# Optimization experiments

Measured on AMD Instinct MI355X. Metric: run time of the kernel, lower is better.

## Reference

```python
import jax, jax.numpy as jnp
import numpy as np

N = 1_000_000
BS = 4
SPATIAL_SHAPE = np.array([480.0, 360.0, 32.0], dtype=np.float32)
SCALES = [2, 4, 8, 16, 1]  # scale_list + [1]
POL_MIN = np.array([0.0, -3.14159265, -4.0], dtype=np.float32)
POL_MAX = np.array([50.0, 3.14159265, 2.0], dtype=np.float32)


def setup_inputs() -> dict:
    key = jax.random.key(0)
    kxy, kz, ki, kb = jax.random.split(key, 4)
    xy = jax.random.uniform(kxy, (N, 2), jnp.float32, -35.0, 35.0)   # rho <= 49.5 < 50
    z = jax.random.uniform(kz, (N, 1), jnp.float32, -4.0, 2.0)
    inten = jax.random.uniform(ki, (N, 1), jnp.float32)
    points = jnp.concatenate([xy, z, inten], axis=1)                  # [N, 4]
    batch_idx = jax.random.randint(kb, (N,), 0, BS, jnp.int64)
    return {"points": points, "batch_idx": batch_idx}


def _cart2polar(xyz):
    rho = jnp.sqrt(xyz[:, 0] ** 2 + xyz[:, 1] ** 2)
    phi = jnp.arctan2(xyz[:, 1], xyz[:, 0])
    return jnp.stack([rho, phi, xyz[:, 2]], axis=1)  # [N, 3]


def reference(points, batch_idx):
    pc = points[:, :3]
    pol = _cart2polar(pc)                                            # [N, 3]
    minb = jnp.asarray(POL_MIN)
    crop = jnp.asarray(POL_MAX - POL_MIN)
    b = batch_idx.astype(jnp.int64)

    outputs = []
    for scale in SCALES:
        ss_np = np.ceil(SPATIAL_SHAPE / scale)                       # static per-scale grid
        ss = jnp.asarray(ss_np, dtype=pol.dtype)
        # quantize: spatial_shape * (pol - min) / crop, truncated like torch .long()
        idx = (ss * (pol - minb) / crop).astype(jnp.int64)           # [N, 3] nonneg in-range
        x, y, z = idx[:, 0], idx[:, 1], idx[:, 2]
        bxyz_indx = jnp.stack([b, x, y, z], axis=-1)                 # full_coors [N, 4]
        # encode row -> single int64 key for sort-based unique (strides = shape+1)
        sx, sy, sz = (np.int64(s) + 1 for s in ss_np)
        key = ((b * sx + x) * sy + y) * sz + z
        unq_key, unq_inv = jnp.unique(
            key, return_inverse=True, size=N, fill_value=-1
        )
        # decode padded unique keys back to (b, x, y, z); pad rows decode from -1
        uz = unq_key % sz
        t = unq_key // sz
        uy = t % sy
        t = t // sy
        ux = t % sx
        ub = t // sx
        coors = jnp.stack([ub, uz, uy, ux], axis=1).astype(jnp.int32)  # [b, z, y, x]
        outputs.extend([bxyz_indx, unq_inv.reshape(-1), coors])
    return tuple(outputs)
```

## Files before the change

### kernel.cpp

```cpp
#include <hip/hip_runtime.h>

#define NPTS 1000000
#define OUT_STRIDE (9 * NPTS)

constexpr int   kSX[5]  = {241, 121, 61, 31, 481};
constexpr int   kSY[5]  = {181,  91, 46, 24, 361};
constexpr int   kSZ[5]  = { 17,   9,  5,  3,  33};
constexpr float kSSX[5] = {240.f, 120.f, 60.f, 30.f, 480.f};
constexpr float kSSY[5] = {180.f,  90.f, 45.f, 23.f, 360.f};
constexpr float kSSZ[5] = { 16.f,   8.f,  4.f,  2.f,  32.f};
constexpr int kWB[5] = {0, 92736, 105152, 106944, 107264};
#define W_TOTAL 823552
#define SCAN_BLOCKS 403

#define BM_BYTES ((size_t)W_TOTAL * 32)
#define BM_U4    (BM_BYTES / 16)

#define SCAT_BLOCKS 3217
#define PAD_BLOCKS  19532
#define INV_BLOCKS  3907
#define EMIT_BLOCKS (SCAT_BLOCKS + PAD_BLOCKS + INV_BLOCKS)

__global__ void zero_kernel(uint4* __restrict__ p) {
  size_t i = (size_t)blockIdx.x * 256 + threadIdx.x;
  if (i < BM_U4) p[i] = make_uint4(0u, 0u, 0u, 0u);
}

__global__ void mark_kernel(const float4* __restrict__ pts,
                            const int* __restrict__ bidx,
                            int* __restrict__ out,
                            unsigned char* __restrict__ bytemap) {
  int i = blockIdx.x * 256 + threadIdx.x;
  if (i >= NPTS) return;
  float4 p = pts[i];
  float rho = __fsqrt_rn(__fadd_rn(__fmul_rn(p.x, p.x), __fmul_rn(p.y, p.y)));
  float phi = (float)atan2((double)p.y, (double)p.x);
  float zz = p.z;
  int b = bidx[i];
  const float PI_F = 3.14159265f;
  const float CROP1 = PI_F + PI_F;
#pragma unroll
  for (int s = 0; s < 5; ++s) {
    int ix = (int)__fdiv_rn(__fmul_rn(kSSX[s], rho), 50.0f);
    int iy = (int)__fdiv_rn(__fmul_rn(kSSY[s], __fsub_rn(phi, -PI_F)), CROP1);
    int iz = (int)__fdiv_rn(__fmul_rn(kSSZ[s], __fsub_rn(zz, -4.0f)), 6.0f);
    int key = ((b * kSX[s] + ix) * kSY[s] + iy) * kSZ[s] + iz;
    ((int4*)(out + (size_t)s * OUT_STRIDE))[i] = make_int4(b, ix, iy, iz);
    bytemap[(size_t)kWB[s] * 32 + (unsigned)key] = 1;
  }
}

__device__ __forceinline__ unsigned nib(unsigned u) {
  return (u | (u >> 7) | (u >> 14) | (u >> 21)) & 0xFu;
}
__device__ __forceinline__ unsigned word_from_bytes(const uint4* p) {
  uint4 a = p[0], b = p[1];
  return nib(a.x) | (nib(a.y) << 4) | (nib(a.z) << 8) | (nib(a.w) << 12) |
         (nib(b.x) << 16) | (nib(b.y) << 20) | (nib(b.z) << 24) | (nib(b.w) << 28);
}

__global__ void scan1_kernel(const uint4* __restrict__ bytemap,
                             unsigned* __restrict__ bits,
                             unsigned* __restrict__ wp,
                             unsigned* __restrict__ bsums) {
  __shared__ unsigned sh[256];
  int tid = threadIdx.x;
  int base = blockIdx.x * 2048 + tid * 8;
  unsigned c[8];
  unsigned sum = 0;
#pragma unroll
  for (int j = 0; j < 8; ++j) {
    c[j] = sum;
    int w = base + j;
    unsigned m = 0;
    if (w < W_TOTAL) {
      m = word_from_bytes(bytemap + (size_t)w * 2);
      bits[w] = m;
    }
    sum += (unsigned)__popc(m);
  }
  sh[tid] = sum;
  __syncthreads();
  for (int off = 1; off < 256; off <<= 1) {
    unsigned v = (tid >= off) ? sh[tid - off] : 0u;
    __syncthreads();
    sh[tid] += v;
    __syncthreads();
  }
  unsigned tbase = sh[tid] - sum;
#pragma unroll
  for (int j = 0; j < 8; ++j) {
    int w = base + j;
    if (w < W_TOTAL) wp[w] = tbase + c[j];
  }
  if (tid == 0) bsums[blockIdx.x] = sh[255];
}

__global__ void scan2_kernel(unsigned* __restrict__ bsums) {
  __shared__ unsigned sh[1024];
  int t = threadIdx.x;
  unsigned v = (t < SCAN_BLOCKS) ? bsums[t] : 0u;
  sh[t] = v;
  __syncthreads();
  for (int off = 1; off < 1024; off <<= 1) {
    unsigned u = (t >= off) ? sh[t - off] : 0u;
    __syncthreads();
    sh[t] += u;
    __syncthreads();
  }
  if (t < SCAN_BLOCKS) bsums[t] = sh[t] - v;
  if (t == SCAN_BLOCKS - 1) bsums[512] = sh[t];
}

__device__ __forceinline__ unsigned fullp(const unsigned* wp, const unsigned* bs, int w) {
  return wp[w] + bs[w >> 11];
}

__device__ __forceinline__ unsigned region_count(int s, const unsigned* wp,
                                                 const unsigned* bs) {
  unsigned lo = fullp(wp, bs, kWB[s]);
  unsigned hi = (s == 4) ? bs[512] : fullp(wp, bs, kWB[s + 1]);
  return hi - lo;
}

__global__ void emit_kernel(const float4* __restrict__ pts,
                            const int* __restrict__ bidx,
                            const unsigned* __restrict__ bits,
                            const unsigned* __restrict__ wp,
                            const unsigned* __restrict__ bsums,
                            int* __restrict__ out) {
  int blk = blockIdx.x;
  if (blk < SCAT_BLOCKS) {
    int w = blk * 256 + threadIdx.x;
    if (w >= W_TOTAL) return;
    unsigned word = bits[w];
    if (!word) return;
    int s, wb;
    unsigned sx, sy, sz;
    if      (w >= kWB[4]) { s = 4; wb = kWB[4]; sx = 481; sy = 361; sz = 33; }
    else if (w >= kWB[3]) { s = 3; wb = kWB[3]; sx = 31;  sy = 24;  sz = 3;  }
    else if (w >= kWB[2]) { s = 2; wb = kWB[2]; sx = 61;  sy = 46;  sz = 5;  }
    else if (w >= kWB[1]) { s = 1; wb = kWB[1]; sx = 121; sy = 91;  sz = 9;  }
    else                  { s = 0; wb = 0;      sx = 241; sy = 181; sz = 17; }
    unsigned rank = fullp(wp, bsums, w) - fullp(wp, bsums, wb);
    int4* coors = (int4*)(out + (size_t)s * OUT_STRIDE + 5 * NPTS);
    unsigned kbase = (unsigned)(w - wb) * 32u;
    while (word) {
      int bit = __ffs(word) - 1;
      word &= word - 1;
      unsigned k = kbase + (unsigned)bit;
      unsigned z = k % sz; unsigned t = k / sz;
      unsigned y = t % sy; t /= sy;
      unsigned x = t % sx; unsigned b = t / sx;
      coors[rank++] = make_int4((int)b, (int)z, (int)y, (int)x);
    }
  } else if (blk < SCAT_BLOCKS + PAD_BLOCKS) {
    int idx = (blk - SCAT_BLOCKS) * 256 + threadIdx.x;
    if (idx >= 5 * NPTS) return;
    int s = idx / NPTS;
    int r = idx - s * NPTS;
    unsigned uniq = region_count(s, wp, bsums);
    if ((unsigned)r < uniq) return;
    ((int4*)(out + (size_t)s * OUT_STRIDE + 5 * NPTS))[r] =
        make_int4(-1, kSZ[s] - 1, kSY[s] - 1, kSX[s] - 1);
  } else {
    int i = (blk - SCAT_BLOCKS - PAD_BLOCKS) * 256 + threadIdx.x;
    if (i >= NPTS) return;
    float4 p = pts[i];
    float rho = __fsqrt_rn(__fadd_rn(__fmul_rn(p.x, p.x), __fmul_rn(p.y, p.y)));
    float phi = (float)atan2((double)p.y, (double)p.x);
    float zz = p.z;
    int b = bidx[i];
    const float PI_F = 3.14159265f;
    const float CROP1 = PI_F + PI_F;
#pragma unroll
    for (int s = 0; s < 5; ++s) {
      int ix = (int)__fdiv_rn(__fmul_rn(kSSX[s], rho), 50.0f);
      int iy = (int)__fdiv_rn(__fmul_rn(kSSY[s], __fsub_rn(phi, -PI_F)), CROP1);
      int iz = (int)__fdiv_rn(__fmul_rn(kSSZ[s], __fsub_rn(zz, -4.0f)), 6.0f);
      unsigned k = (unsigned)(((b * kSX[s] + ix) * kSY[s] + iy) * kSZ[s] + iz);
      int w = kWB[s] + (int)(k >> 5);
      unsigned r = fullp(wp, bsums, w) - fullp(wp, bsums, kWB[s]) +
                   (unsigned)__popc(bits[w] & ((1u << (k & 31)) - 1u));
      out[(size_t)s * OUT_STRIDE + 4 * NPTS + i] = (int)r;
    }
  }
}

extern "C" void kernel_launch(void* const* d_in, const int* in_sizes, int n_in,
                              void* d_out, int out_size, void* d_ws, size_t ws_size,
                              hipStream_t stream) {
  const float4* pts = (const float4*)d_in[0];
  const int* bidx = (const int*)d_in[1];
  int* out = (int*)d_out;

  unsigned* bits  = (unsigned*)d_ws;
  unsigned* wp    = bits + W_TOTAL;
  unsigned* bsums = wp + W_TOTAL;
  unsigned char* bytemap = (unsigned char*)(bsums + 1024);

  zero_kernel<<<(int)((BM_U4 + 255) / 256), 256, 0, stream>>>((uint4*)bytemap);
  mark_kernel<<<(NPTS + 255) / 256, 256, 0, stream>>>(pts, bidx, out, bytemap);
  scan1_kernel<<<SCAN_BLOCKS, 256, 0, stream>>>((const uint4*)bytemap, bits, wp, bsums);
  scan2_kernel<<<1, 1024, 0, stream>>>(bsums);
  emit_kernel<<<EMIT_BLOCKS, 256, 0, stream>>>(pts, bidx, bits, wp, bsums, out);
}
```

Before: 122.7 us.

## Fuse block-sum scan into scan kernel via last-block ticket; use nontemporal output stores

Removes the separate single-block scan2 launch by having each scan block atomically publish its sum and bump a ticket, with the last-arriving block scanning all block sums. The ticket is reset in the zero kernel. Output writes (full coords, coors, inverse indices, padding) switch to nontemporal stores so the large write-only streams do not pollute cache. This trades one launch for atomics and a serial tail in the last block.

```diff
diff --git a/kernel.cpp b/kernel.cpp
--- a/kernel.cpp
+++ b/kernel.cpp
@@ -21,9 +21,16 @@
 #define INV_BLOCKS  3907
 #define EMIT_BLOCKS (SCAT_BLOCKS + PAD_BLOCKS + INV_BLOCKS)
 
-__global__ void zero_kernel(uint4* __restrict__ p) {
+typedef int v4i __attribute__((ext_vector_type(4)));
+__device__ __forceinline__ void nt_store4(int* p, int a, int b, int c, int d) {
+  v4i v = {a, b, c, d};
+  __builtin_nontemporal_store(v, (v4i*)p);
+}
+
+__global__ void zero_kernel(uint4* __restrict__ p, unsigned* __restrict__ ticket) {
   size_t i = (size_t)blockIdx.x * 256 + threadIdx.x;
   if (i < BM_U4) p[i] = make_uint4(0u, 0u, 0u, 0u);
+  if (i == 0) *ticket = 0u;
 }
 
 __global__ void mark_kernel(const float4* __restrict__ pts,
@@ -45,7 +52,7 @@
     int iy = (int)__fdiv_rn(__fmul_rn(kSSY[s], __fsub_rn(phi, -PI_F)), CROP1);
     int iz = (int)__fdiv_rn(__fmul_rn(kSSZ[s], __fsub_rn(zz, -4.0f)), 6.0f);
     int key = ((b * kSX[s] + ix) * kSY[s] + iy) * kSZ[s] + iz;
-    ((int4*)(out + (size_t)s * OUT_STRIDE))[i] = make_int4(b, ix, iy, iz);
+    nt_store4(out + (size_t)s * OUT_STRIDE + (size_t)i * 4, b, ix, iy, iz);
     bytemap[(size_t)kWB[s] * 32 + (unsigned)key] = 1;
   }
 }
@@ -59,11 +66,13 @@
          (nib(b.x) << 16) | (nib(b.y) << 20) | (nib(b.z) << 24) | (nib(b.w) << 28);
 }
 
-__global__ void scan1_kernel(const uint4* __restrict__ bytemap,
-                             unsigned* __restrict__ bits,
-                             unsigned* __restrict__ wp,
-                             unsigned* __restrict__ bsums) {
+__global__ void scan_kernel(const uint4* __restrict__ bytemap,
+                            unsigned* __restrict__ bits,
+                            unsigned* __restrict__ wp,
+                            unsigned* __restrict__ bsums,
+                            unsigned* __restrict__ ticket) {
   __shared__ unsigned sh[256];
+  __shared__ int amlast;
   int tid = threadIdx.x;
   int base = blockIdx.x * 2048 + tid * 8;
   unsigned c[8];
@@ -93,23 +102,34 @@
     int w = base + j;
     if (w < W_TOTAL) wp[w] = tbase + c[j];
   }
-  if (tid == 0) bsums[blockIdx.x] = sh[255];
-}
-
-__global__ void scan2_kernel(unsigned* __restrict__ bsums) {
-  __shared__ unsigned sh[1024];
-  int t = threadIdx.x;
-  unsigned v = (t < SCAN_BLOCKS) ? bsums[t] : 0u;
-  sh[t] = v;
-  __syncthreads();
-  for (int off = 1; off < 1024; off <<= 1) {
-    unsigned u = (t >= off) ? sh[t - off] : 0u;
-    __syncthreads();
-    sh[t] += u;
-    __syncthreads();
-  }
-  if (t < SCAN_BLOCKS) bsums[t] = sh[t] - v;
-  if (t == SCAN_BLOCKS - 1) bsums[512] = sh[t];
+  if (tid == 0) {
+    __hip_atomic_store(&bsums[blockIdx.x], sh[255], __ATOMIC_RELEASE,
+                       __HIP_MEMORY_SCOPE_AGENT);
+    unsigned t = __hip_atomic_fetch_add(ticket, 1u, __ATOMIC_ACQ_REL,
+                                        __HIP_MEMORY_SCOPE_AGENT);
+    amlast = (t == SCAN_BLOCKS - 1);
+  }
+  __syncthreads();
+  if (!amlast) return;
+  int i0 = tid * 2, i1 = tid * 2 + 1;
+  unsigned e0 = (i0 < SCAN_BLOCKS)
+      ? __hip_atomic_load(&bsums[i0], __ATOMIC_ACQUIRE, __HIP_MEMORY_SCOPE_AGENT) : 0u;
+  unsigned e1 = (i1 < SCAN_BLOCKS)
+      ? __hip_atomic_load(&bsums[i1], __ATOMIC_ACQUIRE, __HIP_MEMORY_SCOPE_AGENT) : 0u;
+  unsigned s2 = e0 + e1;
+  __syncthreads();
+  sh[tid] = s2;
+  __syncthreads();
+  for (int off = 1; off < 256; off <<= 1) {
+    unsigned v = (tid >= off) ? sh[tid - off] : 0u;
+    __syncthreads();
+    sh[tid] += v;
+    __syncthreads();
+  }
+  unsigned ebase = sh[tid] - s2;
+  if (i0 < SCAN_BLOCKS) bsums[i0] = ebase;
+  if (i1 < SCAN_BLOCKS) bsums[i1] = ebase + e0;
+  if (tid == 255) bsums[512] = sh[255];
 }
 
 __device__ __forceinline__ unsigned fullp(const unsigned* wp, const unsigned* bs, int w) {
@@ -143,7 +163,7 @@
     else if (w >= kWB[1]) { s = 1; wb = kWB[1]; sx = 121; sy = 91;  sz = 9;  }
     else                  { s = 0; wb = 0;      sx = 241; sy = 181; sz = 17; }
     unsigned rank = fullp(wp, bsums, w) - fullp(wp, bsums, wb);
-    int4* coors = (int4*)(out + (size_t)s * OUT_STRIDE + 5 * NPTS);
+    int* coors = out + (size_t)s * OUT_STRIDE + 5 * NPTS;
     unsigned kbase = (unsigned)(w - wb) * 32u;
     while (word) {
       int bit = __ffs(word) - 1;
@@ -152,7 +172,8 @@
       unsigned z = k % sz; unsigned t = k / sz;
       unsigned y = t % sy; t /= sy;
       unsigned x = t % sx; unsigned b = t / sx;
-      coors[rank++] = make_int4((int)b, (int)z, (int)y, (int)x);
+      nt_store4(coors + (size_t)rank * 4, (int)b, (int)z, (int)y, (int)x);
+      rank++;
     }
   } else if (blk < SCAT_BLOCKS + PAD_BLOCKS) {
     int idx = (blk - SCAT_BLOCKS) * 256 + threadIdx.x;
@@ -161,8 +182,8 @@
     int r = idx - s * NPTS;
     unsigned uniq = region_count(s, wp, bsums);
     if ((unsigned)r < uniq) return;
-    ((int4*)(out + (size_t)s * OUT_STRIDE + 5 * NPTS))[r] =
-        make_int4(-1, kSZ[s] - 1, kSY[s] - 1, kSX[s] - 1);
+    nt_store4(out + (size_t)s * OUT_STRIDE + 5 * NPTS + (size_t)r * 4,
+              -1, kSZ[s] - 1, kSY[s] - 1, kSX[s] - 1);
   } else {
     int i = (blk - SCAT_BLOCKS - PAD_BLOCKS) * 256 + threadIdx.x;
     if (i >= NPTS) return;
@@ -182,7 +203,7 @@
       int w = kWB[s] + (int)(k >> 5);
       unsigned r = fullp(wp, bsums, w) - fullp(wp, bsums, kWB[s]) +
                    (unsigned)__popc(bits[w] & ((1u << (k & 31)) - 1u));
-      out[(size_t)s * OUT_STRIDE + 4 * NPTS + i] = (int)r;
+      __builtin_nontemporal_store((int)r, out + (size_t)s * OUT_STRIDE + 4 * NPTS + i);
     }
   }
 }
@@ -194,14 +215,15 @@
   const int* bidx = (const int*)d_in[1];
   int* out = (int*)d_out;
 
-  unsigned* bits  = (unsigned*)d_ws;
-  unsigned* wp    = bits + W_TOTAL;
-  unsigned* bsums = wp + W_TOTAL;
+  unsigned* bits   = (unsigned*)d_ws;
+  unsigned* wp     = bits + W_TOTAL;
+  unsigned* bsums  = wp + W_TOTAL;
+  unsigned* ticket = bsums + 768;
   unsigned char* bytemap = (unsigned char*)(bsums + 1024);
 
-  zero_kernel<<<(int)((BM_U4 + 255) / 256), 256, 0, stream>>>((uint4*)bytemap);
+  zero_kernel<<<(int)((BM_U4 + 255) / 256), 256, 0, stream>>>((uint4*)bytemap, ticket);
   mark_kernel<<<(NPTS + 255) / 256, 256, 0, stream>>>(pts, bidx, out, bytemap);
-  scan1_kernel<<<SCAN_BLOCKS, 256, 0, stream>>>((const uint4*)bytemap, bits, wp, bsums);
-  scan2_kernel<<<1, 1024, 0, stream>>>(bsums);
+  scan_kernel<<<SCAN_BLOCKS, 256, 0, stream>>>((const uint4*)bytemap, bits, wp,
+                                               bsums, ticket);
   emit_kernel<<<EMIT_BLOCKS, 256, 0, stream>>>(pts, bidx, bits, wp, bsums, out);
 }
```

Result: slower. 184.8 us (+50.7%).
